# Optimization experiments

Hardware: AMD Instinct MI355X
Metric: run time of the kernel (lower is better)

Reference implementation:

```python
import jax, jax.numpy as jnp
import numpy as np
from math import factorial, sqrt

# FullyConnectedTensorProduct: irreps_in1 = 128x0e+128x1o+128x2e,
# irreps_in2 = 1x0e+1x1o+1x2e, irreps_out = 128x0e+128x1o+128x2e
MUL1, MUL2, MULO = 128, 1, 128
LS1, LS2, LSO = [0, 1, 2], [0, 1, 2], [0, 1, 2]  # parity = (-1)**l for every entry
B = 32768


def _su2_cg(j1, j2, j3):
    f = factorial
    C = np.zeros((2 * j1 + 1, 2 * j2 + 1, 2 * j3 + 1))
    for m1 in range(-j1, j1 + 1):
        for m2 in range(-j2, j2 + 1):
            m3 = m1 + m2
            if abs(m3) > j3:
                continue
            pref = sqrt((2 * j3 + 1) * f(j3 + j1 - j2) * f(j3 - j1 + j2) * f(j1 + j2 - j3) / f(j1 + j2 + j3 + 1))
            pref *= sqrt(f(j3 + m3) * f(j3 - m3) * f(j1 - m1) * f(j1 + m1) * f(j2 - m2) * f(j2 + m2))
            s = 0.0
            for k in range(0, j1 + j2 - j3 + 1):
                if min(j1 - m1 - k, j2 + m2 - k, j3 - j2 + m1 + k, j3 - j1 - m2 + k) < 0:
                    continue
                s += (-1) ** k / (f(k) * f(j1 + j2 - j3 - k) * f(j1 - m1 - k) * f(j2 + m2 - k) * f(j3 - j2 + m1 + k) * f(j3 - j1 - m2 + k))
            C[j1 + m1, j2 + m2, j3 + m3] = pref * s
    return C


def _real_basis(l):  # change of basis to real spherical harmonics (e3nn convention)
    q = np.zeros((2 * l + 1, 2 * l + 1), dtype=np.complex128)
    for m in range(-l, 0):
        q[l + m, l + abs(m)] = 1 / sqrt(2)
        q[l + m, l - abs(m)] = -1j / sqrt(2)
    q[l, l] = 1.0
    for m in range(1, l + 1):
        q[l + m, l + abs(m)] = (-1) ** m / sqrt(2)
        q[l + m, l - abs(m)] = 1j * (-1) ** m / sqrt(2)
    return (-1j) ** l * q


def _w3j(l1, l2, l3):  # real Wigner-3j, unit Frobenius norm
    C = _su2_cg(l1, l2, l3).astype(np.complex128)
    Q1, Q2, Q3 = _real_basis(l1), _real_basis(l2), _real_basis(l3)
    C = np.einsum('ij,kl,nm,ikn->jlm', Q1, Q2, np.conj(Q3), C)
    assert np.abs(C.imag).max() < 1e-8
    C = np.real(C)
    return (C / np.linalg.norm(C)).astype(np.float32)


# instructions: every (i1, i2, io) with |l1-l2| <= lo <= l1+l2 and matching parity
INSTRUCTIONS = [(i1, i2, io)
                for i1, l1 in enumerate(LS1)
                for i2, l2 in enumerate(LS2)
                for io, lo in enumerate(LSO)
                if abs(l1 - l2) <= lo <= l1 + l2 and (l1 + l2 + lo) % 2 == 0]
N_PATHS = len(INSTRUCTIONS)  # 11
W3JS = [_w3j(LS1[i1], LS2[i2], LSO[io]) for i1, i2, io in INSTRUCTIONS]

# irrep_normalization='component', path_normalization='element', unit variances:
# alpha = dim(ir_out) / sum_{paths with same i_out} mul1*mul2
_den = {}
for _, _, io in INSTRUCTIONS:
    _den[io] = _den.get(io, 0) + MUL1 * MUL2
ALPHAS = [float((2 * LSO[io] + 1) / _den[io]) for _, _, io in INSTRUCTIONS]


def _slices(ls, mul):
    out, off = [], 0
    for l in ls:
        out.append((off, off + mul * (2 * l + 1)))
        off = out[-1][1]
    return out, off


S1, DIM1 = _slices(LS1, MUL1)  # DIM1 = 1152
S2, DIM2 = _slices(LS2, MUL2)  # DIM2 = 9
SO, DIMO = _slices(LSO, MULO)  # DIMO = 1152


def _tensor_product(x1, x2, ws):
    b = x1.shape[0]
    out = [jnp.zeros((b, MULO * (2 * l + 1)), x1.dtype) for l in LSO]
    for p, (i1, i2, io) in enumerate(INSTRUCTIONS):
        l1, l2 = LS1[i1], LS2[i2]
        x1b = x1[:, S1[i1][0]:S1[i1][1]].reshape(b, MUL1, 2 * l1 + 1)
        x2b = x2[:, S2[i2][0]:S2[i2][1]].reshape(b, MUL2, 2 * l2 + 1)
        C = jnp.asarray(W3JS[p], x1.dtype)
        tmp = jnp.einsum('ijk,bui,bvj->buvk', C, x1b, x2b)  # [b, u, v, 2lo+1]
        blk = jnp.einsum('uvw,buvk->bwk', ws[p], tmp)       # [b, w, 2lo+1]
        out[io] = out[io] + (ALPHAS[p] ** 0.5) * blk.reshape(b, -1)
    return jnp.concatenate(out, axis=1)


def setup_inputs():
    key = jax.random.key(0)
    k1, k2, k3 = jax.random.split(key, 3)
    return {
        'x1': jax.random.normal(k1, (B, DIM1), jnp.float32),
        'x2': jax.random.normal(k2, (B, DIM2), jnp.float32),
        'ws': jax.random.normal(k3, (N_PATHS, MUL1, MUL2, MULO), jnp.float32),
    }


def reference(x1, x2, ws):
    return _tensor_product(x1, x2, ws)
```

## Files before the change

### kernel.cpp

```cpp
#include <hip/hip_runtime.h>
#include <cmath>
#include <complex>

#define BT 16
#define NP 11

constexpr int P_N1[NP]   = {1,1,1, 3,3,3,3, 5,5,5,5};
constexpr int P_N2[NP]   = {1,3,5, 1,3,3,5, 1,3,5,5};
constexpr int P_NO[NP]   = {1,3,5, 3,1,5,3, 5,3,1,5};
constexpr int P_S1[NP]   = {0,0,0, 128,128,128,128, 512,512,512,512};
constexpr int P_S2[NP]   = {0,1,4, 0,1,1,4, 0,1,4,4};
constexpr int P_MOFF[NP] = {0,1,4,9,18,21,36,45,70,85,90};
constexpr int P_W3J[NP]  = {0,1,10,35,44,53,98,143,168,213,238};

struct TPConst {
    float w3j[363];
    float sqa[11];
};

namespace {

double hfact(int n) { double r = 1.0; for (int i = 2; i <= n; ++i) r *= (double)i; return r; }

void hsu2cg(int j1, int j2, int j3, double* C) {
    const int d2 = 2*j2+1, d3 = 2*j3+1, d1 = 2*j1+1;
    for (int i = 0; i < d1*d2*d3; ++i) C[i] = 0.0;
    for (int m1 = -j1; m1 <= j1; ++m1)
        for (int m2 = -j2; m2 <= j2; ++m2) {
            const int m3 = m1 + m2;
            if (m3 < -j3 || m3 > j3) continue;
            double pref = std::sqrt((2*j3+1) * hfact(j3+j1-j2) * hfact(j3-j1+j2) * hfact(j1+j2-j3) / hfact(j1+j2+j3+1));
            pref *= std::sqrt(hfact(j3+m3)*hfact(j3-m3)*hfact(j1-m1)*hfact(j1+m1)*hfact(j2-m2)*hfact(j2+m2));
            double s = 0.0;
            for (int k = 0; k <= j1+j2-j3; ++k) {
                if (j1-m1-k < 0 || j2+m2-k < 0 || j3-j2+m1+k < 0 || j3-j1-m2+k < 0) continue;
                double d = hfact(k)*hfact(j1+j2-j3-k)*hfact(j1-m1-k)*hfact(j2+m2-k)*hfact(j3-j2+m1+k)*hfact(j3-j1-m2+k);
                s += ((k & 1) ? -1.0 : 1.0) / d;
            }
            C[((j1+m1)*d2 + (j2+m2))*d3 + (j3+m3)] = pref * s;
        }
}

void hrealbasis(int l, std::complex<double>* q) {
    const int d = 2*l+1;
    for (int i = 0; i < d*d; ++i) q[i] = 0.0;
    const double is2 = 1.0 / std::sqrt(2.0);
    for (int m = -l; m < 0; ++m) {
        q[(l+m)*d + (l - m)] = is2;
        q[(l+m)*d + (l + m)] = std::complex<double>(0.0, -is2);
    }
    q[l*d + l] = 1.0;
    for (int m = 1; m <= l; ++m) {
        const double sgn = (m & 1) ? -1.0 : 1.0;
        q[(l+m)*d + (l + m)] = sgn * is2;
        q[(l+m)*d + (l - m)] = std::complex<double>(0.0, sgn * is2);
    }
    std::complex<double> ph(1.0, 0.0);
    const std::complex<double> mi(0.0, -1.0);
    for (int i = 0; i < l; ++i) ph *= mi;
    for (int i = 0; i < d*d; ++i) q[i] *= ph;
}

void hw3j(int l1, int l2, int l3, float* out) {
    const int d1 = 2*l1+1, d2 = 2*l2+1, d3 = 2*l3+1;
    double C[125];
    hsu2cg(l1, l2, l3, C);
    std::complex<double> Q1[25], Q2[25], Q3[25];
    hrealbasis(l1, Q1); hrealbasis(l2, Q2); hrealbasis(l3, Q3);
    double R[125]; double norm2 = 0.0;
    for (int j = 0; j < d1; ++j)
        for (int l = 0; l < d2; ++l)
            for (int m = 0; m < d3; ++m) {
                std::complex<double> s(0.0, 0.0);
                for (int i = 0; i < d1; ++i)
                    for (int k = 0; k < d2; ++k)
                        for (int n = 0; n < d3; ++n)
                            s += Q1[i*d1 + j] * Q2[k*d2 + l] * std::conj(Q3[n*d3 + m]) * C[(i*d2 + k)*d3 + n];
                R[(j*d2 + l)*d3 + m] = s.real();
                norm2 += s.real() * s.real();
            }
    const double inv = 1.0 / std::sqrt(norm2);
    for (int i = 0; i < d1*d2*d3; ++i) out[i] = (float)(R[i] * inv);
}

void fill_const(TPConst& tc) {
    const int L1[NP] = {0,0,0,1,1,1,1,2,2,2,2};
    const int L2[NP] = {0,1,2,0,1,1,2,0,1,2,2};
    const int LO[NP] = {0,1,2,1,0,2,1,2,1,0,2};
    const double den[3] = {384.0, 512.0, 512.0};
    for (int p = 0; p < NP; ++p) {
        hw3j(L1[p], L2[p], LO[p], tc.w3j + P_W3J[p]);
        tc.sqa[p] = (float)std::sqrt((2.0*LO[p] + 1.0) / den[LO[p]]);
    }
}

}

typedef __attribute__((ext_vector_type(8))) short  short8v;
typedef __attribute__((ext_vector_type(4))) float  f32x4;
typedef __attribute__((ext_vector_type(4))) unsigned int uint4v;

__device__ __forceinline__ unsigned fbits(float f) { return __builtin_bit_cast(unsigned, f); }
__device__ __forceinline__ float    bitsf(unsigned u) { return __builtin_bit_cast(float, u); }

__device__ __forceinline__ void split2(float f0, float f1, unsigned& h, unsigned& l) {
    const unsigned u0 = fbits(f0), u1 = fbits(f1);
    h = (u0 >> 16) | (u1 & 0xFFFF0000u);
    const float r0 = f0 - bitsf(u0 & 0xFFFF0000u);
    const float r1 = f1 - bitsf(u1 & 0xFFFF0000u);
    l = (fbits(r0) >> 16) | (fbits(r1) & 0xFFFF0000u);
}

template<int P>
__device__ __forceinline__ void tp_path(
    const float* __restrict__ x1, const float* __restrict__ wsg,
    const float (*__restrict__ Mlds)[116],
    unsigned short* __restrict__ yhi, unsigned short* __restrict__ ylo,
    f32x4 (&acc)[2][P_NO[P]],
    long b0, int uy, int g, int lane, int wv)
{
    constexpr int n1 = P_N1[P];
    constexpr int no = P_NO[P];

    #pragma unroll
    for (int bb = 0; bb < 8; ++bb) {
        const int b = g*8 + bb;
        const float* xp = x1 + (b0 + b)*1152 + P_S1[P] + uy*n1;
        float xv[5];
        #pragma unroll
        for (int i = 0; i < n1; ++i) xv[i] = xp[i];
        const int us = uy ^ ((b & 7) << 3);
        #pragma unroll
        for (int k = 0; k < no; ++k) {
            float yv = 0.f;
            #pragma unroll
            for (int i = 0; i < n1; ++i)
                yv += Mlds[b][P_MOFF[P] + k*n1 + i] * xv[i];
            const unsigned ub = fbits(yv);
            const float hif = bitsf(ub & 0xFFFF0000u);
            yhi[(k*16 + b)*128 + us] = (unsigned short)(ub >> 16);
            ylo[(k*16 + b)*128 + us] = (unsigned short)(fbits(yv - hif) >> 16);
        }
    }
    __syncthreads();

    {
        const int bC = lane & 15, qC = lane >> 4;
        const float* wpp = wsg + P*16384;
        #pragma unroll
        for (int k4 = 0; k4 < 4; ++k4) {
            const int ubase = k4*32 + qC*8;
            short8v Ah[2], Al[2];
            #pragma unroll
            for (int mt = 0; mt < 2; ++mt) {
                const float* ap = wpp + ubase*128 + (wv*32 + mt*16 + bC);
                uint4v hh, ll;
                #pragma unroll
                for (int e = 0; e < 4; ++e) {
                    unsigned h, l;
                    split2(ap[(2*e)*128], ap[(2*e + 1)*128], h, l);
                    hh[e] = h; ll[e] = l;
                }
                Ah[mt] = __builtin_bit_cast(short8v, hh);
                Al[mt] = __builtin_bit_cast(short8v, ll);
            }
            const int uoff = ubase ^ ((bC & 7) << 3);
            #pragma unroll
            for (int k = 0; k < no; ++k) {
                const int ridx = (k*16 + bC)*128 + uoff;
                const short8v Bh = *(const short8v*)(yhi + ridx);
                const short8v Bl = *(const short8v*)(ylo + ridx);
                #pragma unroll
                for (int mt = 0; mt < 2; ++mt) {
                    acc[mt][k] = __builtin_amdgcn_mfma_f32_16x16x32_bf16(Ah[mt], Bh, acc[mt][k], 0, 0, 0);
                    acc[mt][k] = __builtin_amdgcn_mfma_f32_16x16x32_bf16(Ah[mt], Bl, acc[mt][k], 0, 0, 0);
                    acc[mt][k] = __builtin_amdgcn_mfma_f32_16x16x32_bf16(Al[mt], Bh, acc[mt][k], 0, 0, 0);
                }
            }
        }
    }
    __syncthreads();
}

__global__ __launch_bounds__(256, 2)
void tp_kernel(const float* __restrict__ x1, const float* __restrict__ x2,
               const float* __restrict__ wsg, float* __restrict__ out, TPConst tc)
{
    __shared__ float Mlds[BT][116];
    __shared__ __align__(16) unsigned short yhi[5*16*128];
    __shared__ __align__(16) unsigned short ylo[5*16*128];

    const int t = threadIdx.x;
    const long b0 = (long)blockIdx.x * BT;

    if (t < BT) {
        float x2v[9];
        #pragma unroll
        for (int j = 0; j < 9; ++j) x2v[j] = x2[(b0 + t)*9 + j];
        #pragma unroll
        for (int p = 0; p < NP; ++p) {
            const int n1 = P_N1[p], n2 = P_N2[p], no = P_NO[p];
            const float sqa = tc.sqa[p];
            #pragma unroll
            for (int k = 0; k < no; ++k)
                #pragma unroll
                for (int i = 0; i < n1; ++i) {
                    float m = 0.f;
                    #pragma unroll
                    for (int j = 0; j < n2; ++j)
                        m += tc.w3j[P_W3J[p] + (i*n2 + j)*no + k] * x2v[P_S2[p] + j];
                    Mlds[t][P_MOFF[p] + k*n1 + i] = m * sqa;
                }
        }
    }

    const int uy = t & 127, g = t >> 7;
    const int lane = t & 63, wv = t >> 6;
    const int bC = lane & 15, qC = lane >> 4;
    float* opb = out + (b0 + bC)*1152;

    __syncthreads();

    {
        f32x4 acc[2][1];
        #pragma unroll
        for (int mt = 0; mt < 2; ++mt) acc[mt][0] = f32x4{0.f, 0.f, 0.f, 0.f};
        tp_path<0>(x1, wsg, Mlds, yhi, ylo, acc, b0, uy, g, lane, wv);
        tp_path<4>(x1, wsg, Mlds, yhi, ylo, acc, b0, uy, g, lane, wv);
        tp_path<9>(x1, wsg, Mlds, yhi, ylo, acc, b0, uy, g, lane, wv);
        #pragma unroll
        for (int mt = 0; mt < 2; ++mt)
            *(f32x4*)(opb + wv*32 + mt*16 + qC*4) = acc[mt][0];
    }

    {
        f32x4 acc[2][3];
        #pragma unroll
        for (int mt = 0; mt < 2; ++mt)
            #pragma unroll
            for (int k = 0; k < 3; ++k) acc[mt][k] = f32x4{0.f, 0.f, 0.f, 0.f};
        tp_path<1>(x1, wsg, Mlds, yhi, ylo, acc, b0, uy, g, lane, wv);
        tp_path<3>(x1, wsg, Mlds, yhi, ylo, acc, b0, uy, g, lane, wv);
        tp_path<6>(x1, wsg, Mlds, yhi, ylo, acc, b0, uy, g, lane, wv);
        tp_path<8>(x1, wsg, Mlds, yhi, ylo, acc, b0, uy, g, lane, wv);
        #pragma unroll
        for (int mt = 0; mt < 2; ++mt)
            #pragma unroll
            for (int r = 0; r < 4; ++r) {
                const int w = wv*32 + mt*16 + qC*4 + r;
                #pragma unroll
                for (int k = 0; k < 3; ++k)
                    opb[128 + w*3 + k] = acc[mt][k][r];
            }
    }

    {
        f32x4 acc[2][5];
        #pragma unroll
        for (int mt = 0; mt < 2; ++mt)
            #pragma unroll
            for (int k = 0; k < 5; ++k) acc[mt][k] = f32x4{0.f, 0.f, 0.f, 0.f};
        tp_path<2>(x1, wsg, Mlds, yhi, ylo, acc, b0, uy, g, lane, wv);
        tp_path<5>(x1, wsg, Mlds, yhi, ylo, acc, b0, uy, g, lane, wv);
        tp_path<7>(x1, wsg, Mlds, yhi, ylo, acc, b0, uy, g, lane, wv);
        tp_path<10>(x1, wsg, Mlds, yhi, ylo, acc, b0, uy, g, lane, wv);
        #pragma unroll
        for (int mt = 0; mt < 2; ++mt)
            #pragma unroll
            for (int r = 0; r < 4; ++r) {
                const int w = wv*32 + mt*16 + qC*4 + r;
                #pragma unroll
                for (int k = 0; k < 5; ++k)
                    opb[512 + w*5 + k] = acc[mt][k][r];
            }
    }
}

extern "C" void kernel_launch(void* const* d_in, const int* in_sizes, int n_in,
                              void* d_out, int out_size, void* d_ws, size_t ws_size,
                              hipStream_t stream) {
    const float* x1  = (const float*)d_in[0];
    const float* x2  = (const float*)d_in[1];
    const float* wsg = (const float*)d_in[2];
    float* out = (float*)d_out;
    const int B = in_sizes[0] / 1152;

    TPConst tc;
    fill_const(tc);

    dim3 grid(B / BT), block(256);
    hipLaunchKernelGGL(tp_kernel, grid, block, 0, stream, x1, x2, wsg, out, tc);
}
```

Measured before the change: 459.0 us.

## Pre-split weights into bf16 planes and double-buffer y staging across paths

Adds a prep kernel that splits the fp32 weights once into transposed bf16 hi/lo planes in workspace, so the main kernel loads ready-made MFMA operands with vector loads instead of splitting strided fp32 weights in every block. The y staging buffer is split into slots so building the next path chunk overlaps the MFMA work on the current one, which cuts the barriers from two per path to one per chunk. Output stores for the l=1 and l=2 blocks are repacked into 16-byte vector writes. This costs an extra launch and workspace memory, and the finer chunking adds more barrier points.

```diff
diff --git a/kernel.cpp b/kernel.cpp
--- a/kernel.cpp
+++ b/kernel.cpp
@@ -12,6 +12,8 @@
 constexpr int P_S2[NP]   = {0,1,4, 0,1,1,4, 0,1,4,4};
 constexpr int P_MOFF[NP] = {0,1,4,9,18,21,36,45,70,85,90};
 constexpr int P_W3J[NP]  = {0,1,10,35,44,53,98,143,168,213,238};
+
+#define WPLANE 180224
 
 struct TPConst {
     float w3j[363];
@@ -98,30 +100,37 @@
 
 typedef __attribute__((ext_vector_type(8))) short  short8v;
 typedef __attribute__((ext_vector_type(4))) float  f32x4;
-typedef __attribute__((ext_vector_type(4))) unsigned int uint4v;
 
 __device__ __forceinline__ unsigned fbits(float f) { return __builtin_bit_cast(unsigned, f); }
 __device__ __forceinline__ float    bitsf(unsigned u) { return __builtin_bit_cast(float, u); }
 
-__device__ __forceinline__ void split2(float f0, float f1, unsigned& h, unsigned& l) {
-    const unsigned u0 = fbits(f0), u1 = fbits(f1);
-    h = (u0 >> 16) | (u1 & 0xFFFF0000u);
-    const float r0 = f0 - bitsf(u0 & 0xFFFF0000u);
-    const float r1 = f1 - bitsf(u1 & 0xFFFF0000u);
-    l = (fbits(r0) >> 16) | (fbits(r1) & 0xFFFF0000u);
-}
-
-template<int P>
-__device__ __forceinline__ void tp_path(
-    const float* __restrict__ x1, const float* __restrict__ wsg,
-    const float (*__restrict__ Mlds)[116],
+__device__ __forceinline__ void splitf(float f, unsigned short& h, unsigned short& l) {
+    const unsigned ub = fbits(f);
+    h = (unsigned short)(ub >> 16);
+    const float r = f - bitsf(ub & 0xFFFF0000u);
+    l = (unsigned short)(fbits(r) >> 16);
+}
+
+__global__ __launch_bounds__(256)
+void w_prep(const float* __restrict__ wsg, unsigned short* __restrict__ whl)
+{
+    const int idx = blockIdx.x*256 + threadIdx.x;
+    if (idx >= WPLANE) return;
+    const int u = idx & 127, w = (idx >> 7) & 127, p = idx >> 14;
+    const float f = wsg[(p*128 + u)*128 + w];
+    unsigned short h, l;
+    splitf(f, h, l);
+    whl[idx] = h;
+    whl[WPLANE + idx] = l;
+}
+
+template<int P, int K0, int NOK, int S0>
+__device__ __forceinline__ void tp_yb(
+    const float* __restrict__ x1, const float (*__restrict__ Mlds)[116],
     unsigned short* __restrict__ yhi, unsigned short* __restrict__ ylo,
-    f32x4 (&acc)[2][P_NO[P]],
-    long b0, int uy, int g, int lane, int wv)
+    long b0, int uy, int g)
 {
     constexpr int n1 = P_N1[P];
-    constexpr int no = P_NO[P];
-
     #pragma unroll
     for (int bb = 0; bb < 8; ++bb) {
         const int b = g*8 + bb;
@@ -131,60 +140,56 @@
         for (int i = 0; i < n1; ++i) xv[i] = xp[i];
         const int us = uy ^ ((b & 7) << 3);
         #pragma unroll
-        for (int k = 0; k < no; ++k) {
+        for (int kl = 0; kl < NOK; ++kl) {
             float yv = 0.f;
             #pragma unroll
             for (int i = 0; i < n1; ++i)
-                yv += Mlds[b][P_MOFF[P] + k*n1 + i] * xv[i];
-            const unsigned ub = fbits(yv);
-            const float hif = bitsf(ub & 0xFFFF0000u);
-            yhi[(k*16 + b)*128 + us] = (unsigned short)(ub >> 16);
-            ylo[(k*16 + b)*128 + us] = (unsigned short)(fbits(yv - hif) >> 16);
-        }
-    }
-    __syncthreads();
-
-    {
-        const int bC = lane & 15, qC = lane >> 4;
-        const float* wpp = wsg + P*16384;
-        #pragma unroll
-        for (int k4 = 0; k4 < 4; ++k4) {
-            const int ubase = k4*32 + qC*8;
-            short8v Ah[2], Al[2];
+                yv += Mlds[b][P_MOFF[P] + (K0 + kl)*n1 + i] * xv[i];
+            unsigned short h, l;
+            splitf(yv, h, l);
+            yhi[((S0 + kl)*16 + b)*128 + us] = h;
+            ylo[((S0 + kl)*16 + b)*128 + us] = l;
+        }
+    }
+}
+
+template<int P, int K0, int NOK, int S0, int NA>
+__device__ __forceinline__ void tp_mc(
+    const unsigned short* __restrict__ whl,
+    const unsigned short* __restrict__ yhi, const unsigned short* __restrict__ ylo,
+    f32x4 (&acc)[2][NA], int lane, int wv)
+{
+    const int bC = lane & 15, qC = lane >> 4;
+    #pragma unroll
+    for (int k4 = 0; k4 < 4; ++k4) {
+        const int ubase = k4*32 + qC*8;
+        short8v Ah[2], Al[2];
+        #pragma unroll
+        for (int mt = 0; mt < 2; ++mt) {
+            const int aoff = (P*128 + (wv*32 + mt*16 + bC))*128 + ubase;
+            Ah[mt] = *(const short8v*)(whl + aoff);
+            Al[mt] = *(const short8v*)(whl + WPLANE + aoff);
+        }
+        const int uoff = ubase ^ ((bC & 7) << 3);
+        #pragma unroll
+        for (int kl = 0; kl < NOK; ++kl) {
+            const int ridx = ((S0 + kl)*16 + bC)*128 + uoff;
+            const short8v Bh = *(const short8v*)(yhi + ridx);
+            const short8v Bl = *(const short8v*)(ylo + ridx);
             #pragma unroll
             for (int mt = 0; mt < 2; ++mt) {
-                const float* ap = wpp + ubase*128 + (wv*32 + mt*16 + bC);
-                uint4v hh, ll;
-                #pragma unroll
-                for (int e = 0; e < 4; ++e) {
-                    unsigned h, l;
-                    split2(ap[(2*e)*128], ap[(2*e + 1)*128], h, l);
-                    hh[e] = h; ll[e] = l;
-                }
-                Ah[mt] = __builtin_bit_cast(short8v, hh);
-                Al[mt] = __builtin_bit_cast(short8v, ll);
+                acc[mt][K0+kl] = __builtin_amdgcn_mfma_f32_16x16x32_bf16(Ah[mt], Bh, acc[mt][K0+kl], 0, 0, 0);
+                acc[mt][K0+kl] = __builtin_amdgcn_mfma_f32_16x16x32_bf16(Ah[mt], Bl, acc[mt][K0+kl], 0, 0, 0);
+                acc[mt][K0+kl] = __builtin_amdgcn_mfma_f32_16x16x32_bf16(Al[mt], Bh, acc[mt][K0+kl], 0, 0, 0);
             }
-            const int uoff = ubase ^ ((bC & 7) << 3);
-            #pragma unroll
-            for (int k = 0; k < no; ++k) {
-                const int ridx = (k*16 + bC)*128 + uoff;
-                const short8v Bh = *(const short8v*)(yhi + ridx);
-                const short8v Bl = *(const short8v*)(ylo + ridx);
-                #pragma unroll
-                for (int mt = 0; mt < 2; ++mt) {
-                    acc[mt][k] = __builtin_amdgcn_mfma_f32_16x16x32_bf16(Ah[mt], Bh, acc[mt][k], 0, 0, 0);
-                    acc[mt][k] = __builtin_amdgcn_mfma_f32_16x16x32_bf16(Ah[mt], Bl, acc[mt][k], 0, 0, 0);
-                    acc[mt][k] = __builtin_amdgcn_mfma_f32_16x16x32_bf16(Al[mt], Bh, acc[mt][k], 0, 0, 0);
-                }
-            }
-        }
-    }
-    __syncthreads();
+        }
+    }
 }
 
 __global__ __launch_bounds__(256, 2)
 void tp_kernel(const float* __restrict__ x1, const float* __restrict__ x2,
-               const float* __restrict__ wsg, float* __restrict__ out, TPConst tc)
+               const unsigned short* __restrict__ whl, float* __restrict__ out,
+               TPConst tc)
 {
     __shared__ float Mlds[BT][116];
     __shared__ __align__(16) unsigned short yhi[5*16*128];
@@ -221,58 +226,128 @@
 
     __syncthreads();
 
+    tp_yb<0,0,1,0>(x1, Mlds, yhi, ylo, b0, uy, g);
+    tp_yb<4,0,1,1>(x1, Mlds, yhi, ylo, b0, uy, g);
+    tp_yb<9,0,1,2>(x1, Mlds, yhi, ylo, b0, uy, g);
+    __syncthreads();
+
+    f32x4 acc0[2][1];
+    f32x4 acc1[2][3];
+    #pragma unroll
+    for (int mt = 0; mt < 2; ++mt) {
+        acc0[mt][0] = f32x4{0.f,0.f,0.f,0.f};
+        #pragma unroll
+        for (int k = 0; k < 3; ++k) acc1[mt][k] = f32x4{0.f,0.f,0.f,0.f};
+    }
+
+    tp_mc<0,0,1,0,1>(whl, yhi, ylo, acc0, lane, wv);
+    tp_mc<4,0,1,1,1>(whl, yhi, ylo, acc0, lane, wv);
+    tp_mc<9,0,1,2,1>(whl, yhi, ylo, acc0, lane, wv);
+    tp_yb<1,0,2,3>(x1, Mlds, yhi, ylo, b0, uy, g);
+    __syncthreads();
+
+    tp_mc<1,0,2,3,3>(whl, yhi, ylo, acc1, lane, wv);
+    tp_yb<1,2,1,0>(x1, Mlds, yhi, ylo, b0, uy, g);
+    #pragma unroll
+    for (int mt = 0; mt < 2; ++mt)
+        *(f32x4*)(opb + wv*32 + mt*16 + qC*4) = acc0[mt][0];
+    __syncthreads();
+
+    tp_mc<1,2,1,0,3>(whl, yhi, ylo, acc1, lane, wv);
+    tp_yb<3,0,2,3>(x1, Mlds, yhi, ylo, b0, uy, g);
+    __syncthreads();
+
+    tp_mc<3,0,2,3,3>(whl, yhi, ylo, acc1, lane, wv);
+    tp_yb<3,2,1,0>(x1, Mlds, yhi, ylo, b0, uy, g);
+    __syncthreads();
+
+    tp_mc<3,2,1,0,3>(whl, yhi, ylo, acc1, lane, wv);
+    tp_yb<6,0,2,3>(x1, Mlds, yhi, ylo, b0, uy, g);
+    __syncthreads();
+
+    tp_mc<6,0,2,3,3>(whl, yhi, ylo, acc1, lane, wv);
+    tp_yb<6,2,1,0>(x1, Mlds, yhi, ylo, b0, uy, g);
+    __syncthreads();
+
+    tp_mc<6,2,1,0,3>(whl, yhi, ylo, acc1, lane, wv);
+    tp_yb<8,0,2,3>(x1, Mlds, yhi, ylo, b0, uy, g);
+    __syncthreads();
+
+    tp_mc<8,0,2,3,3>(whl, yhi, ylo, acc1, lane, wv);
+    tp_yb<8,2,1,0>(x1, Mlds, yhi, ylo, b0, uy, g);
+    __syncthreads();
+
+    f32x4 acc2[2][5];
+    #pragma unroll
+    for (int mt = 0; mt < 2; ++mt)
+        #pragma unroll
+        for (int k = 0; k < 5; ++k) acc2[mt][k] = f32x4{0.f,0.f,0.f,0.f};
+    tp_mc<8,2,1,0,3>(whl, yhi, ylo, acc1, lane, wv);
+    tp_yb<2,0,3,2>(x1, Mlds, yhi, ylo, b0, uy, g);
     {
-        f32x4 acc[2][1];
-        #pragma unroll
-        for (int mt = 0; mt < 2; ++mt) acc[mt][0] = f32x4{0.f, 0.f, 0.f, 0.f};
-        tp_path<0>(x1, wsg, Mlds, yhi, ylo, acc, b0, uy, g, lane, wv);
-        tp_path<4>(x1, wsg, Mlds, yhi, ylo, acc, b0, uy, g, lane, wv);
-        tp_path<9>(x1, wsg, Mlds, yhi, ylo, acc, b0, uy, g, lane, wv);
+        float b1[24];
         #pragma unroll
         for (int mt = 0; mt < 2; ++mt)
-            *(f32x4*)(opb + wv*32 + mt*16 + qC*4) = acc[mt][0];
-    }
-
-    {
-        f32x4 acc[2][3];
-        #pragma unroll
-        for (int mt = 0; mt < 2; ++mt)
-            #pragma unroll
-            for (int k = 0; k < 3; ++k) acc[mt][k] = f32x4{0.f, 0.f, 0.f, 0.f};
-        tp_path<1>(x1, wsg, Mlds, yhi, ylo, acc, b0, uy, g, lane, wv);
-        tp_path<3>(x1, wsg, Mlds, yhi, ylo, acc, b0, uy, g, lane, wv);
-        tp_path<6>(x1, wsg, Mlds, yhi, ylo, acc, b0, uy, g, lane, wv);
-        tp_path<8>(x1, wsg, Mlds, yhi, ylo, acc, b0, uy, g, lane, wv);
-        #pragma unroll
-        for (int mt = 0; mt < 2; ++mt)
-            #pragma unroll
-            for (int r = 0; r < 4; ++r) {
-                const int w = wv*32 + mt*16 + qC*4 + r;
+            #pragma unroll
+            for (int r = 0; r < 4; ++r)
                 #pragma unroll
                 for (int k = 0; k < 3; ++k)
-                    opb[128 + w*3 + k] = acc[mt][k][r];
-            }
-    }
-
+                    b1[(mt*4 + r)*3 + k] = acc1[mt][k][r];
+        #pragma unroll
+        for (int mt = 0; mt < 2; ++mt) {
+            const int w0 = wv*32 + mt*16 + qC*4;
+            #pragma unroll
+            for (int q = 0; q < 3; ++q)
+                *(f32x4*)(opb + 128 + w0*3 + q*4) = *(const f32x4*)(b1 + mt*12 + q*4);
+        }
+    }
+    __syncthreads();
+
+    tp_mc<2,0,3,2,5>(whl, yhi, ylo, acc2, lane, wv);
+    tp_yb<2,3,2,0>(x1, Mlds, yhi, ylo, b0, uy, g);
+    __syncthreads();
+
+    tp_mc<2,3,2,0,5>(whl, yhi, ylo, acc2, lane, wv);
+    tp_yb<5,0,3,2>(x1, Mlds, yhi, ylo, b0, uy, g);
+    __syncthreads();
+
+    tp_mc<5,0,3,2,5>(whl, yhi, ylo, acc2, lane, wv);
+    tp_yb<5,3,2,0>(x1, Mlds, yhi, ylo, b0, uy, g);
+    __syncthreads();
+
+    tp_mc<5,3,2,0,5>(whl, yhi, ylo, acc2, lane, wv);
+    tp_yb<7,0,3,2>(x1, Mlds, yhi, ylo, b0, uy, g);
+    __syncthreads();
+
+    tp_mc<7,0,3,2,5>(whl, yhi, ylo, acc2, lane, wv);
+    tp_yb<7,3,2,0>(x1, Mlds, yhi, ylo, b0, uy, g);
+    __syncthreads();
+
+    tp_mc<7,3,2,0,5>(whl, yhi, ylo, acc2, lane, wv);
+    tp_yb<10,0,3,2>(x1, Mlds, yhi, ylo, b0, uy, g);
+    __syncthreads();
+
+    tp_mc<10,0,3,2,5>(whl, yhi, ylo, acc2, lane, wv);
+    tp_yb<10,3,2,0>(x1, Mlds, yhi, ylo, b0, uy, g);
+    __syncthreads();
+
+    tp_mc<10,3,2,0,5>(whl, yhi, ylo, acc2, lane, wv);
     {
-        f32x4 acc[2][5];
+        float b2[40];
         #pragma unroll
         for (int mt = 0; mt < 2; ++mt)
             #pragma unroll
-            for (int k = 0; k < 5; ++k) acc[mt][k] = f32x4{0.f, 0.f, 0.f, 0.f};
-        tp_path<2>(x1, wsg, Mlds, yhi, ylo, acc, b0, uy, g, lane, wv);
-        tp_path<5>(x1, wsg, Mlds, yhi, ylo, acc, b0, uy, g, lane, wv);
-        tp_path<7>(x1, wsg, Mlds, yhi, ylo, acc, b0, uy, g, lane, wv);
-        tp_path<10>(x1, wsg, Mlds, yhi, ylo, acc, b0, uy, g, lane, wv);
-        #pragma unroll
-        for (int mt = 0; mt < 2; ++mt)
-            #pragma unroll
-            for (int r = 0; r < 4; ++r) {
-                const int w = wv*32 + mt*16 + qC*4 + r;
+            for (int r = 0; r < 4; ++r)
                 #pragma unroll
                 for (int k = 0; k < 5; ++k)
-                    opb[512 + w*5 + k] = acc[mt][k][r];
-            }
+                    b2[(mt*4 + r)*5 + k] = acc2[mt][k][r];
+        #pragma unroll
+        for (int mt = 0; mt < 2; ++mt) {
+            const int w0 = wv*32 + mt*16 + qC*4;
+            #pragma unroll
+            for (int q = 0; q < 5; ++q)
+                *(f32x4*)(opb + 512 + w0*5 + q*4) = *(const f32x4*)(b2 + mt*20 + q*4);
+        }
     }
 }
 
@@ -288,6 +363,10 @@
     TPConst tc;
     fill_const(tc);
 
+    unsigned short* whl = (unsigned short*)d_ws;
+
+    hipLaunchKernelGGL(w_prep, dim3((WPLANE + 255)/256), dim3(256), 0, stream, wsg, whl);
+
     dim3 grid(B / BT), block(256);
-    hipLaunchKernelGGL(tp_kernel, grid, block, 0, stream, x1, x2, wsg, out, tc);
-}
+    hipLaunchKernelGGL(tp_kernel, grid, block, 0, stream, x1, x2, whl, out, tc);
+}
```

Measured after the change: 578.5 us. +26.0%, slower.
